# Optimization experiments

Hardware: AMD Instinct MI355X
Metric: run time of the kernel (lower is better)

The kernel has to match this reference:

```python
import jax, jax.numpy as jnp
import numpy as np

H = 256          # NUM_HIDDEN_NODES
D = 2 * H        # encoder feature dim
C_CLS = 1000     # NUM_CLASSES
B = 16
S = 1024
STEPS = 8
WINDOW = 4
MIN_VAL = 1e-8   # min_val global in original


def moving_sum(x, back, fwd):
    # x: [B, T]; sum over window [i-back, i+fwd] (zero padded), as conv1d with ones kernel
    xp = jnp.pad(x, ((0, 0), (back, fwd)))
    k = jnp.ones((1, 1, back + fwd + 1), x.dtype)
    y = jax.lax.conv_general_dilated(xp[:, None, :], k, window_strides=(1,),
                                     padding='VALID', dimension_numbers=('NCH', 'OIH', 'NCH'))
    return y[:, 0, :]


def setup_inputs() -> dict:
    key = jax.random.key(0)
    ks = jax.random.split(key, 24)
    def lin(k, i, o):
        return jax.random.normal(k, (i, o), jnp.float32) * np.float32(1.0 / np.sqrt(i))
    def vec(k, n):
        return jax.random.normal(k, (n,), jnp.float32) * np.float32(1.0 / np.sqrt(n))
    return {
        'enc_output': jax.random.normal(ks[0], (B, S, D), jnp.float32),
        'target': jax.random.randint(ks[1], (B, STEPS), 0, C_CLS),
        'length_enc': jax.random.randint(ks[2], (B,), S // 2, S + 1),
        'noise': jax.random.normal(ks[3], (STEPS, B, S), jnp.float32),
        'Ws_mono_w': lin(ks[4], H, D), 'Ws_mono_b': jnp.zeros((D,), jnp.float32),
        'Wh_mono': lin(ks[5], D, D),
        'v_mono': vec(ks[6], D),
        'g_mono': jnp.full((1,), 1.0 / np.sqrt(D), jnp.float32),
        'r_mono': jnp.full((1,), -4.0, jnp.float32),
        'Ws_chunk_w': lin(ks[7], H, D), 'Ws_chunk_b': jnp.zeros((D,), jnp.float32),
        'Wh_chunk': lin(ks[8], D, D),
        'v_chunk': vec(ks[9], D),
        'L_sy': lin(ks[10], H, H),
        'L_gy_w': lin(ks[11], D, H), 'L_gy_b': jnp.zeros((H,), jnp.float32),
        'L_yy_w': lin(ks[12], H, C_CLS), 'L_yy_b': jnp.zeros((C_CLS,), jnp.float32),
        'L_ys': jax.random.normal(ks[13], (C_CLS, 4 * H), jnp.float32) * 0.02,
        'L_ss': lin(ks[14], H, 4 * H),
        'L_gs_w': lin(ks[15], D, 4 * H), 'L_gs_b': jnp.zeros((4 * H,), jnp.float32),
    }


def reference(enc_output, target, length_enc, noise,
              Ws_mono_w, Ws_mono_b, Wh_mono, v_mono, g_mono, r_mono,
              Ws_chunk_w, Ws_chunk_b, Wh_chunk, v_chunk,
              L_sy, L_gy_w, L_gy_b, L_yy_w, L_yy_b, L_ys, L_ss, L_gs_w, L_gs_b):
    Bn, Sn, _ = enc_output.shape
    Hn = L_sy.shape[0]
    mask = jnp.arange(Sn)[None, :] >= length_enc[:, None]   # True = padded
    neg_inf = jnp.float32(-jnp.inf)
    # step-invariant encoder projections (hoisted out of decode loop)
    enc_mono = enc_output @ Wh_mono     # [B,S,D]
    enc_chunk = enc_output @ Wh_chunk   # [B,S,D]
    v_norm = g_mono[0] / jnp.linalg.norm(v_mono)

    def step(carry, xs):
        s, c, a_prev = carry
        nz, tgt = xs
        # monotonic energies
        tmp1 = jnp.tanh(enc_mono + (s @ Ws_mono_w + Ws_mono_b)[:, None, :])
        e_mono = jnp.einsum('bsd,d->bs', v_norm * tmp1, v_mono) + r_mono[0]
        e_mono = jnp.where(mask, neg_inf, e_mono)
        p = jax.nn.sigmoid(e_mono + nz)
        # monotonic attention recurrence via stable cumsum/cumprod
        logf = jnp.log(jnp.clip(1.0 - p[:, :-1], MIN_VAL, 1.0))
        cpp = jnp.concatenate([jnp.ones((Bn, 1), p.dtype), jnp.exp(jnp.cumsum(logf, axis=1))], axis=1)
        q = cpp * jnp.cumsum(a_prev / jnp.clip(cpp, MIN_VAL, 1.0), axis=1)
        alpha = jnp.clip(p * q, MIN_VAL, 1.0)
        # chunkwise attention
        tmp2 = jnp.tanh(enc_chunk + (s @ Ws_chunk_w + Ws_chunk_b)[:, None, :])
        e_ch = jnp.where(mask, neg_inf, jnp.einsum('bsd,d->bs', tmp2, v_chunk))
        e_ch = e_ch - jnp.max(e_ch, axis=1, keepdims=True)
        ex = jnp.clip(jnp.exp(e_ch), 1e-5, None)
        denom = jnp.clip(moving_sum(ex, WINDOW - 1, 0), 1e-10, None)
        beta = ex * moving_sum(alpha / denom, 0, WINDOW - 1)
        ctx = jnp.einsum('bs,bsd->bd', beta, enc_output)
        # decoder LSTM cell
        rec = L_ys[tgt] + s @ L_ss + ctx @ L_gs_w + L_gs_b
        i, f, g, o = jnp.split(rec, 4, axis=1)
        c_new = jax.nn.sigmoid(f) * c + jax.nn.sigmoid(i) * jnp.tanh(g)
        s_new = jax.nn.sigmoid(o) * jnp.tanh(c_new)
        y = jnp.tanh(ctx @ L_gy_w + L_gy_b + s_new @ L_sy) @ L_yy_w + L_yy_b
        return (s_new, c_new, jax.lax.stop_gradient(alpha)), y

    a0 = jnp.zeros((Bn, Sn), enc_output.dtype).at[:, 0].set(1.0)
    s0 = jnp.zeros((Bn, Hn), enc_output.dtype)
    c0 = jnp.zeros((Bn, Hn), enc_output.dtype)
    _, ys = jax.lax.scan(step, (s0, c0, a0), (noise, target.T))
    return jnp.transpose(ys, (1, 0, 2))   # [B, steps, NUM_CLASSES]
```

## Files before the change

kernel.cpp:

```cpp
#include <hip/hip_runtime.h>
#include <math.h>
#include <float.h>

#define HN 256
#define DN 512
#define CCLS 1000
#define BB 16
#define SS 1024
#define NSTEPS 8
#define G4 1024
#define KV 768

using f16x8 = __attribute__((ext_vector_type(8))) _Float16;
using f32x4 = __attribute__((ext_vector_type(4))) float;

__device__ __forceinline__ void gload_lds16(const void* g, void* l) {
    __builtin_amdgcn_global_load_lds((const __attribute__((address_space(1))) void*)g,
                                     (__attribute__((address_space(3))) void*)l, 16, 0, 0);
}

__device__ __forceinline__ float ftanh(float x) {
    float e = __expf(2.f * x);
    return 1.f - 2.f / (e + 1.f);
}
__device__ __forceinline__ float fsigm(float x) {
    return 1.f / (1.f + __expf(-x));
}

__global__ __launch_bounds__(512) void init_k(const float* __restrict__ vM, const float* __restrict__ g,
                                              const float* __restrict__ Wsmb, const float* __restrict__ Wscb,
                                              float* __restrict__ aA, float* __restrict__ sctxA,
                                              float* __restrict__ cbuf,
                                              float* __restrict__ smb, float* __restrict__ scb,
                                              float* __restrict__ vn) {
    int bid = blockIdx.x, t = threadIdx.x;
    if (bid == 96) {
        __shared__ float red[512];
        float x = vM[t];
        red[t] = x * x;
        __syncthreads();
        for (int off = 256; off > 0; off >>= 1) {
            if (t < off) red[t] += red[t + off];
            __syncthreads();
        }
        if (t == 0) vn[0] = g[0] / sqrtf(red[0]);
        return;
    }
    int i = bid * 512 + t;
    if (i < 16384) {
        aA[i] = ((i & (SS - 1)) == 0) ? 1.f : 0.f;
    } else if (i < 28672) {
        sctxA[i - 16384] = 0.f;
    } else if (i < 32768) {
        cbuf[i - 28672] = 0.f;
    } else if (i < 40960) {
        int j = i - 32768;
        smb[j] = Wsmb[j & (DN - 1)];
    } else {
        int j = i - 40960;
        scb[j] = Wscb[j & (DN - 1)];
    }
}

__global__ __launch_bounds__(256) void conv_enc_k(const float* __restrict__ in,
                                                  _Float16* __restrict__ out) {
    size_t i = ((size_t)blockIdx.x * 256 + threadIdx.x) * 8;
    float4 a = *(const float4*)(in + i);
    float4 b = *(const float4*)(in + i + 4);
    f16x8 o;
    o[0] = (_Float16)a.x; o[1] = (_Float16)a.y; o[2] = (_Float16)a.z; o[3] = (_Float16)a.w;
    o[4] = (_Float16)b.x; o[5] = (_Float16)b.y; o[6] = (_Float16)b.z; o[7] = (_Float16)b.w;
    *(f16x8*)(out + i) = o;
}

__global__ __launch_bounds__(256) void convW_k(const float* __restrict__ W1,
                                               const float* __restrict__ W2,
                                               _Float16* __restrict__ WcT) {
    int kt = blockIdx.x;
    int nt = blockIdx.y;
    __shared__ _Float16 tile[32][33];
    int tx = threadIdx.x & 31, ty = threadIdx.x >> 5;
    int n0 = nt * 32, k0 = kt * 32;
    for (int r = 0; r < 32; r += 8) {
        int k = k0 + ty + r, n = n0 + tx;
        float v = (n < 512) ? W1[(size_t)k * 512 + n] : W2[(size_t)k * 512 + (n - 512)];
        tile[tx][ty + r] = (_Float16)v;
    }
    __syncthreads();
    for (int r = 0; r < 32; r += 8) {
        int n = n0 + ty + r, k = k0 + tx;
        WcT[(size_t)n * 512 + k] = tile[ty + r][tx];
    }
}

__global__ __launch_bounds__(256) void transAll_k(const float* __restrict__ Lss, const float* __restrict__ Lgs,
                                                  const float* __restrict__ Lsy, const float* __restrict__ Lgy,
                                                  const float* __restrict__ Wsm, const float* __restrict__ Wsc,
                                                  const float* __restrict__ Lyy,
                                                  float* __restrict__ WgT, float* __restrict__ WyT,
                                                  float* __restrict__ WpT, float* __restrict__ LyyT) {
    int bid = blockIdx.x;
    const float* src; float* dst; int R, C, dstride, coloff, ctiles;
    if (bid < 256)       { src = Lss; dst = WgT;  R = 256; C = 1024; dstride = KV; coloff = 0;  ctiles = 32; }
    else if (bid < 768)  { src = Lgs; dst = WgT;  R = 512; C = 1024; dstride = KV; coloff = HN; ctiles = 32; bid -= 256; }
    else if (bid < 832)  { src = Lsy; dst = WyT;  R = 256; C = 256;  dstride = KV; coloff = 0;  ctiles = 8;  bid -= 768; }
    else if (bid < 960)  { src = Lgy; dst = WyT;  R = 512; C = 256;  dstride = KV; coloff = HN; ctiles = 8;  bid -= 832; }
    else if (bid < 1088) { src = Wsm; dst = WpT;  R = 256; C = 512;  dstride = HN; coloff = 0;  ctiles = 16; bid -= 960; }
    else if (bid < 1216) { src = Wsc; dst = WpT + (size_t)DN * HN; R = 256; C = 512; dstride = HN; coloff = 0; ctiles = 16; bid -= 1088; }
    else                 { src = Lyy; dst = LyyT; R = 256; C = 1000; dstride = HN; coloff = 0;  ctiles = 32; bid -= 1216; }
    int ct = bid % ctiles, rt = bid / ctiles;
    __shared__ float tile[32][33];
    int c0 = ct * 32, r0 = rt * 32;
    int tx = threadIdx.x & 31, ty = threadIdx.x >> 5;
    for (int rr = 0; rr < 32; rr += 8) {
        int r = r0 + ty + rr, cc = c0 + tx;
        tile[ty + rr][tx] = (r < R && cc < C) ? src[(size_t)r * C + cc] : 0.f;
    }
    __syncthreads();
    for (int rr = 0; rr < 32; rr += 8) {
        int cc = c0 + ty + rr, r = r0 + tx;
        if (cc < C && r < R) dst[(size_t)cc * dstride + coloff + r] = tile[tx][ty + rr];
    }
}

__global__ __launch_bounds__(256) void gemm16_k(const _Float16* __restrict__ A16,
                                                const _Float16* __restrict__ WcT,
                                                _Float16* __restrict__ encMC) {
    __shared__ _Float16 Alds[128 * 32];
    __shared__ _Float16 Blds[128 * 32];
    int bm = blockIdx.x;
    int bn = blockIdx.y;
    int tid = threadIdx.x;
    int lane = tid & 63;
    int w = tid >> 6;
    int wr = w >> 1, wc = w & 1;
    int lr = lane & 15;
    int kg = lane >> 4;
    f32x4 acc[4][4];
#pragma unroll
    for (int i = 0; i < 4; i++)
#pragma unroll
        for (int j = 0; j < 4; j++) acc[i][j] = (f32x4){0.f, 0.f, 0.f, 0.f};

    int wavebase = tid & ~63;
    for (int k0 = 0; k0 < 512; k0 += 32) {
        __syncthreads();
#pragma unroll
        for (int is = 0; is < 2; is++) {
            int l = is * 256 + tid;
            int row = l >> 2, kgs = l & 3;
            int kp = kgs ^ ((row ^ (row >> 2)) & 3);
            gload_lds16(A16 + (size_t)(bm * 128 + row) * 512 + k0 + kp * 8,
                        (char*)Alds + (size_t)(is * 256 + wavebase) * 16);
            gload_lds16(WcT + (size_t)(bn * 128 + row) * 512 + k0 + kp * 8,
                        (char*)Blds + (size_t)(is * 256 + wavebase) * 16);
        }
        __syncthreads();
        f16x8 af[4], bf[4];
#pragma unroll
        for (int mi = 0; mi < 4; mi++) {
            int r = wr * 64 + mi * 16 + lr;
            int kp = kg ^ ((r ^ (r >> 2)) & 3);
            af[mi] = *(const f16x8*)(Alds + r * 32 + kp * 8);
        }
#pragma unroll
        for (int ni = 0; ni < 4; ni++) {
            int cgl = wc * 64 + ni * 16 + lr;
            int kp = kg ^ ((cgl ^ (cgl >> 2)) & 3);
            bf[ni] = *(const f16x8*)(Blds + cgl * 32 + kp * 8);
        }
#pragma unroll
        for (int mi = 0; mi < 4; mi++)
#pragma unroll
            for (int ni = 0; ni < 4; ni++)
                acc[mi][ni] = __builtin_amdgcn_mfma_f32_16x16x32_f16(af[mi], bf[ni], acc[mi][ni], 0, 0, 0);
    }
    int cr = lane >> 4;
#pragma unroll
    for (int mi = 0; mi < 4; mi++)
#pragma unroll
        for (int ni = 0; ni < 4; ni++) {
            int col = bn * 128 + wc * 64 + ni * 16 + lr;
#pragma unroll
            for (int j = 0; j < 4; j++) {
                int row = bm * 128 + wr * 64 + mi * 16 + cr * 4 + j;
                encMC[(size_t)row * 1024 + col] = (_Float16)acc[mi][ni][j];
            }
        }
}

__device__ __forceinline__ void out_proj(int bid2, int tid, float* shbuf,
                                         const float* __restrict__ yv,
                                         const float* __restrict__ LyyT, const float* __restrict__ Lyyb,
                                         float* __restrict__ out, int tt) {
    for (int i = tid * 4; i < BB * HN; i += 1024)
        *(float4*)&shbuf[i] = *(const float4*)&yv[i];
    __syncthreads();
    int wave = tid >> 6, lane = tid & 63;
    int c0 = (bid2 * 4 + wave) * 4;
    for (int q = 0; q < 4; q++) {
        int cc = c0 + q;
        if (cc >= CCLS) break;
        const float* wp = LyyT + (size_t)cc * HN;
        float acc[BB] = {0.f};
#pragma unroll
        for (int k = 0; k < 4; k++) {
            int e = lane + k * 64;
            float wv = wp[e];
#pragma unroll
            for (int b = 0; b < BB; b++) acc[b] = fmaf(wv, shbuf[b * HN + e], acc[b]);
        }
#pragma unroll
        for (int b = 0; b < BB; b++)
#pragma unroll
            for (int off = 32; off > 0; off >>= 1) acc[b] += __shfl_xor(acc[b], off);
        if (lane == 0) {
            float bias = Lyyb[cc];
#pragma unroll
            for (int b = 0; b < BB; b++) out[((size_t)b * NSTEPS + tt) * CCLS + cc] = acc[b] + bias;
        }
    }
}

__global__ __launch_bounds__(256) void energy_out_k(const _Float16* __restrict__ encMC,
                                                    const float* __restrict__ sm, const float* __restrict__ sc,
                                                    const float* __restrict__ vM, const float* __restrict__ vC,
                                                    const float* __restrict__ vnorm, const float* __restrict__ rmono,
                                                    const int* __restrict__ len, const float* __restrict__ noise_t,
                                                    float* __restrict__ p, float* __restrict__ ech,
                                                    const float* __restrict__ yv,
                                                    const float* __restrict__ LyyT, const float* __restrict__ Lyyb,
                                                    float* __restrict__ out, int t) {
    __shared__ float shbuf[BB * HN];
    int tid = threadIdx.x;
    if (blockIdx.x >= 4096) {
        if (t > 0) out_proj(blockIdx.x - 4096, tid, shbuf, yv, LyyT, Lyyb, out, t - 1);
        return;
    }
    int wave = blockIdx.x * 4 + (tid >> 6);
    int lane = tid & 63;
    int b = wave >> 10;
    int si = wave & 1023;
    const f16x8* row = (const f16x8*)(encMC + (size_t)wave * 1024);
    f16x8 em = row[lane];
    f16x8 ec = row[64 + lane];
    int d0 = lane * 8;
    float4 sma = *(const float4*)&sm[b * DN + d0];
    float4 smbv = *(const float4*)&sm[b * DN + d0 + 4];
    float4 sca = *(const float4*)&sc[b * DN + d0];
    float4 scbv = *(const float4*)&sc[b * DN + d0 + 4];
    float4 vma = *(const float4*)&vM[d0];
    float4 vmb = *(const float4*)&vM[d0 + 4];
    float4 vca = *(const float4*)&vC[d0];
    float4 vcb = *(const float4*)&vC[d0 + 4];
    float smv[8] = {sma.x, sma.y, sma.z, sma.w, smbv.x, smbv.y, smbv.z, smbv.w};
    float scv[8] = {sca.x, sca.y, sca.z, sca.w, scbv.x, scbv.y, scbv.z, scbv.w};
    float vmv[8] = {vma.x, vma.y, vma.z, vma.w, vmb.x, vmb.y, vmb.z, vmb.w};
    float vcv[8] = {vca.x, vca.y, vca.z, vca.w, vcb.x, vcb.y, vcb.z, vcb.w};
    float s1 = 0.f, s2 = 0.f;
#pragma unroll
    for (int j = 0; j < 8; j++) {
        s1 += ftanh((float)em[j] + smv[j]) * vmv[j];
        s2 += ftanh((float)ec[j] + scv[j]) * vcv[j];
    }
#pragma unroll
    for (int off = 32; off > 0; off >>= 1) {
        s1 += __shfl_xor(s1, off);
        s2 += __shfl_xor(s2, off);
    }
    if (lane == 0) {
        bool masked = (si >= len[b]);
        float pe;
        if (masked) {
            pe = 0.f;
        } else {
            float e = vnorm[0] * s1 + rmono[0] + noise_t[b * SS + si];
            pe = fsigm(e);
        }
        p[b * SS + si] = pe;
        ech[b * SS + si] = masked ? -INFINITY : s2;
    }
}

__global__ __launch_bounds__(1024) void scanrow_k(const float* __restrict__ p,
                                                  const float* __restrict__ aprev,
                                                  const float* __restrict__ ech,
                                                  float* __restrict__ anew,
                                                  float* __restrict__ beta) {
    int b = blockIdx.x;
    int i = threadIdx.x;
    int lane = i & 63, w = i >> 6;
    __shared__ float wred[16];
    __shared__ float wred2[16];
    __shared__ float mred[16];
    __shared__ float exS[SS];
    __shared__ float rS[SS];
    float pi = p[b * SS + i];
    float lf = (i < SS - 1) ? logf(fminf(fmaxf(1.f - pi, 1e-8f), 1.f)) : 0.f;
    float x = lf;
#pragma unroll
    for (int off = 1; off < 64; off <<= 1) {
        float n = __shfl_up(x, off);
        if (lane >= off) x += n;
    }
    if (lane == 63) wred[w] = x;
    float e = ech[b * SS + i];
    float mx = e;
#pragma unroll
    for (int off = 32; off > 0; off >>= 1) mx = fmaxf(mx, __shfl_xor(mx, off));
    if (lane == 0) mred[w] = mx;
    __syncthreads();
    float base = 0.f;
    for (int j = 0; j < 16; j++)
        if (j < w) base += wred[j];
    float csum = base + x;
    float cpp = expf(csum - lf);
    float u = aprev[b * SS + i] / fminf(fmaxf(cpp, 1e-8f), 1.f);
    float m = mred[0];
    for (int j = 1; j < 16; j++) m = fmaxf(m, mred[j]);
    float x2 = u;
#pragma unroll
    for (int off = 1; off < 64; off <<= 1) {
        float n = __shfl_up(x2, off);
        if (lane >= off) x2 += n;
    }
    if (lane == 63) wred2[w] = x2;
    __syncthreads();
    float base2 = 0.f;
    for (int j = 0; j < 16; j++)
        if (j < w) base2 += wred2[j];
    float q = cpp * (base2 + x2);
    float alpha = fminf(fmaxf(pi * q, 1e-8f), 1.f);
    anew[b * SS + i] = alpha;
    float ex = fmaxf(expf(e - m), 1e-5f);
    exS[i] = ex;
    __syncthreads();
    float denom = ex;
    if (i >= 1) denom += exS[i - 1];
    if (i >= 2) denom += exS[i - 2];
    if (i >= 3) denom += exS[i - 3];
    denom = fmaxf(denom, 1e-10f);
    rS[i] = alpha / denom;
    __syncthreads();
    float bsum = rS[i];
    if (i + 1 < SS) bsum += rS[i + 1];
    if (i + 2 < SS) bsum += rS[i + 2];
    if (i + 3 < SS) bsum += rS[i + 3];
    beta[b * SS + i] = ex * bsum;
}

__global__ __launch_bounds__(512) void ctxpart_k(const float* __restrict__ beta,
                                                 const _Float16* __restrict__ enc16,
                                                 float* __restrict__ part4) {
    int b = blockIdx.x, chunk = blockIdx.y;
    int d = threadIdx.x;
    int s0 = chunk * 256;
    float acc0 = 0.f, acc1 = 0.f;
    const _Float16* eb = enc16 + ((size_t)(b * SS + s0)) * DN + d;
    const float* bb_ = beta + b * SS + s0;
#pragma unroll 4
    for (int s = 0; s < 256; s += 2) {
        acc0 = fmaf(bb_[s], (float)eb[(size_t)s * DN], acc0);
        acc1 = fmaf(bb_[s + 1], (float)eb[(size_t)(s + 1) * DN], acc1);
    }
    part4[((size_t)b * 4 + chunk) * DN + d] = acc0 + acc1;
}

__global__ __launch_bounds__(256) void gl_k(const float* __restrict__ part4,
                                            const float* __restrict__ sIn,
                                            const float* __restrict__ WgT,
                                            const int* __restrict__ target, int t,
                                            const float* __restrict__ Lys, const float* __restrict__ Lgsb,
                                            float* __restrict__ c, float* __restrict__ sOut) {
    __shared__ float sl[BB * KV];
    __shared__ float recL[2][4][BB];
    int tid = threadIdx.x;
    for (int i = tid; i < BB * HN; i += 256) {
        int b = i >> 8, d = i & (HN - 1);
        sl[b * KV + d] = sIn[b * KV + d];
    }
    for (int i = tid; i < BB * DN; i += 256) {
        int b = i >> 9, d = i & (DN - 1);
        const float* pp = part4 + ((size_t)b * 4) * DN + d;
        sl[b * KV + HN + d] = (pp[0] + pp[DN]) + (pp[2 * DN] + pp[3 * DN]);
    }
    __syncthreads();
    int wave = tid >> 6, lane = tid & 63;
    int h0 = blockIdx.x * 2;
    const float* w0p = WgT + (size_t)(h0 + wave * HN) * KV;
    const float* w1p = WgT + (size_t)(h0 + 1 + wave * HN) * KV;
    float acc0[BB] = {0.f}, acc1[BB] = {0.f};
#pragma unroll
    for (int j = 0; j < 12; j++) {
        int e = lane + j * 64;
        float w0 = w0p[e], w1 = w1p[e];
#pragma unroll
        for (int b = 0; b < BB; b++) {
            float xv = sl[b * KV + e];
            acc0[b] = fmaf(w0, xv, acc0[b]);
            acc1[b] = fmaf(w1, xv, acc1[b]);
        }
    }
#pragma unroll
    for (int b = 0; b < BB; b++)
#pragma unroll
        for (int off = 32; off > 0; off >>= 1) {
            acc0[b] += __shfl_xor(acc0[b], off);
            acc1[b] += __shfl_xor(acc1[b], off);
        }
    if (lane == 0) {
#pragma unroll
        for (int b = 0; b < BB; b++) {
            recL[0][wave][b] = acc0[b];
            recL[1][wave][b] = acc1[b];
        }
    }
    __syncthreads();
    if (tid < 32) {
        int b = tid & 15, hh = tid >> 4;
        int h = h0 + hh;
        int tgt = target[b * NSTEPS + t];
        const float* ys = Lys + (size_t)tgt * G4;
        float ri = recL[hh][0][b] + ys[h] + Lgsb[h];
        float rf = recL[hh][1][b] + ys[h + HN] + Lgsb[h + HN];
        float rg = recL[hh][2][b] + ys[h + 2 * HN] + Lgsb[h + 2 * HN];
        float ro = recL[hh][3][b] + ys[h + 3 * HN] + Lgsb[h + 3 * HN];
        float cn = fsigm(rf) * c[b * HN + h] + fsigm(ri) * ftanh(rg);
        float sn = fsigm(ro) * ftanh(cn);
        c[b * HN + h] = cn;
        sOut[b * KV + h] = sn;
    }
    if (blockIdx.x == 0) {
        for (int i = tid; i < BB * DN; i += 256) {
            int b = i >> 9, d = i & (DN - 1);
            sOut[b * KV + HN + d] = sl[b * KV + HN + d];
        }
    }
}

__global__ __launch_bounds__(256) void ypj_k(const float* __restrict__ sctx,
                                             const float* __restrict__ WyT, const float* __restrict__ Lgyb,
                                             const float* __restrict__ WpT,
                                             const float* __restrict__ Wsmb, const float* __restrict__ Wscb,
                                             float* __restrict__ yv,
                                             float* __restrict__ smb, float* __restrict__ scb) {
    __shared__ float sl[BB * KV];
    int tid = threadIdx.x;
    for (int i = tid * 4; i < BB * KV; i += 1024)
        *(float4*)&sl[i] = *(const float4*)&sctx[i];
    __syncthreads();
    int wave = tid >> 6, lane = tid & 63;
    if (blockIdx.x < 16) {
        int h0 = blockIdx.x * 16 + wave * 4;
        for (int q = 0; q < 4; q++) {
            int h = h0 + q;
            const float* wp = WyT + (size_t)h * KV;
            float acc[BB] = {0.f};
#pragma unroll
            for (int j = 0; j < 12; j++) {
                int e = lane + j * 64;
                float wv = wp[e];
#pragma unroll
                for (int b = 0; b < BB; b++) acc[b] = fmaf(wv, sl[b * KV + e], acc[b]);
            }
#pragma unroll
            for (int b = 0; b < BB; b++)
#pragma unroll
                for (int off = 32; off > 0; off >>= 1) acc[b] += __shfl_xor(acc[b], off);
            if (lane == 0) {
#pragma unroll
                for (int b = 0; b < BB; b++) yv[b * HN + h] = ftanh(acc[b] + Lgyb[h]);
            }
        }
    } else {
        int j0 = (blockIdx.x - 16) * 16 + wave * 4;
        for (int q = 0; q < 4; q++) {
            int jc = j0 + q;
            const float* wp = WpT + (size_t)jc * HN;
            float acc[BB] = {0.f};
#pragma unroll
            for (int k = 0; k < 4; k++) {
                int e = lane + k * 64;
                float wv = wp[e];
#pragma unroll
                for (int b = 0; b < BB; b++) acc[b] = fmaf(wv, sl[b * KV + e], acc[b]);
            }
#pragma unroll
            for (int b = 0; b < BB; b++)
#pragma unroll
                for (int off = 32; off > 0; off >>= 1) acc[b] += __shfl_xor(acc[b], off);
            if (lane == 0) {
                if (jc < DN) {
#pragma unroll
                    for (int b = 0; b < BB; b++) smb[b * DN + jc] = acc[b] + Wsmb[jc];
                } else {
                    int jj = jc - DN;
#pragma unroll
                    for (int b = 0; b < BB; b++) scb[b * DN + jj] = acc[b] + Wscb[jj];
                }
            }
        }
    }
}

__global__ __launch_bounds__(256) void out_k(const float* __restrict__ yv,
                                             const float* __restrict__ LyyT, const float* __restrict__ Lyyb,
                                             float* __restrict__ out, int t) {
    __shared__ float shbuf[BB * HN];
    out_proj(blockIdx.x, threadIdx.x, shbuf, yv, LyyT, Lyyb, out, t);
}

extern "C" void kernel_launch(void* const* d_in, const int* in_sizes, int n_in,
                              void* d_out, int out_size, void* d_ws, size_t ws_size,
                              hipStream_t stream) {
    const float* enc  = (const float*)d_in[0];
    const int*   target = (const int*)d_in[1];
    const int*   len  = (const int*)d_in[2];
    const float* noise = (const float*)d_in[3];
    const float* Wsm  = (const float*)d_in[4];
    const float* Wsmb = (const float*)d_in[5];
    const float* WhM  = (const float*)d_in[6];
    const float* vM   = (const float*)d_in[7];
    const float* g    = (const float*)d_in[8];
    const float* rm   = (const float*)d_in[9];
    const float* Wsc  = (const float*)d_in[10];
    const float* Wscb = (const float*)d_in[11];
    const float* WhC  = (const float*)d_in[12];
    const float* vC   = (const float*)d_in[13];
    const float* Lsy  = (const float*)d_in[14];
    const float* Lgy  = (const float*)d_in[15];
    const float* Lgyb = (const float*)d_in[16];
    const float* Lyy  = (const float*)d_in[17];
    const float* Lyyb = (const float*)d_in[18];
    const float* Lys  = (const float*)d_in[19];
    const float* Lss  = (const float*)d_in[20];
    const float* Lgs  = (const float*)d_in[21];
    const float* Lgsb = (const float*)d_in[22];
    float* out = (float*)d_out;

    char* w = (char*)d_ws;
    size_t off = 0;
    auto alloc = [&](size_t bytes) { void* pp = w + off; off += (bytes + 255) & ~(size_t)255; return pp; };
    _Float16* A16   = (_Float16*)alloc((size_t)BB * SS * DN * 2);
    _Float16* WcT   = (_Float16*)alloc((size_t)1024 * 512 * 2);
    _Float16* encMC = (_Float16*)alloc((size_t)BB * SS * 1024 * 2);
    float* WgT  = (float*)alloc((size_t)G4 * KV * 4);
    float* WyT  = (float*)alloc((size_t)HN * KV * 4);
    float* WpT  = (float*)alloc((size_t)G4 * HN * 4);
    float* LyyT = (float*)alloc((size_t)CCLS * HN * 4);
    float* smb   = (float*)alloc(BB * DN * 4);
    float* scb   = (float*)alloc(BB * DN * 4);
    float* pbuf  = (float*)alloc(BB * SS * 4);
    float* ech   = (float*)alloc(BB * SS * 4);
    float* aA    = (float*)alloc(BB * SS * 4);
    float* aBf   = (float*)alloc(BB * SS * 4);
    float* betab = (float*)alloc(BB * SS * 4);
    float* part4 = (float*)alloc((size_t)BB * 4 * DN * 4);
    float* sctxA = (float*)alloc((size_t)BB * KV * 4);
    float* sctxB = (float*)alloc((size_t)BB * KV * 4);
    float* yvb   = (float*)alloc((size_t)BB * HN * 4);
    float* cbuf  = (float*)alloc(BB * HN * 4);
    float* vn    = (float*)alloc(16);
    (void)ws_size; (void)in_sizes; (void)n_in; (void)out_size;

    init_k<<<97, 512, 0, stream>>>(vM, g, Wsmb, Wscb, aA, sctxA, cbuf, smb, scb, vn);
    conv_enc_k<<<4096, 256, 0, stream>>>(enc, A16);
    convW_k<<<dim3(16, 32), 256, 0, stream>>>(WhM, WhC, WcT);
    gemm16_k<<<dim3(128, 8), 256, 0, stream>>>(A16, WcT, encMC);
    transAll_k<<<1472, 256, 0, stream>>>(Lss, Lgs, Lsy, Lgy, Wsm, Wsc, Lyy, WgT, WyT, WpT, LyyT);

    for (int t = 0; t < NSTEPS; t++) {
        float* ain  = (t % 2 == 0) ? aA : aBf;
        float* aout = (t % 2 == 0) ? aBf : aA;
        float* sIn  = (t % 2 == 0) ? sctxA : sctxB;
        float* sOut = (t % 2 == 0) ? sctxB : sctxA;
        energy_out_k<<<4159, 256, 0, stream>>>(encMC, smb, scb, vM, vC, vn, rm,
                                               len, noise + (size_t)t * BB * SS, pbuf, ech,
                                               yvb, LyyT, Lyyb, out, t);
        scanrow_k<<<BB, 1024, 0, stream>>>(pbuf, ain, ech, aout, betab);
        ctxpart_k<<<dim3(BB, 4), 512, 0, stream>>>(betab, A16, part4);
        gl_k<<<128, 256, 0, stream>>>(part4, sIn, WgT, target, t, Lys, Lgsb, cbuf, sOut);
        ypj_k<<<80, 256, 0, stream>>>(sOut, WyT, Lgyb, WpT, Wsmb, Wscb, yvb, smb, scb);
    }
    out_k<<<63, 256, 0, stream>>>(yvb, LyyT, Lyyb, out, NSTEPS - 1);
}
```

Measured before the change: 563.1 us.

## Fuse context reduction into scan kernel and split state/context buffers

Merges the per-step context weighted-sum into the alpha/beta scan kernel, so beta stays in shared memory and one launch plus the partial-sum buffer go away. The hidden state and context are kept in separate buffers, and gl_k is retiled to 512-thread blocks computing four hidden units each. The fused reduction runs on only 16 blocks with long sequential loops over the sequence, which lowers parallelism for that stage.

New measurement: 768.0 us. 36.4% more time.

```diff
diff --git a/kernel.cpp b/kernel.cpp
--- a/kernel.cpp
+++ b/kernel.cpp
@@ -29,12 +29,12 @@
 
 __global__ __launch_bounds__(512) void init_k(const float* __restrict__ vM, const float* __restrict__ g,
                                               const float* __restrict__ Wsmb, const float* __restrict__ Wscb,
-                                              float* __restrict__ aA, float* __restrict__ sctxA,
+                                              float* __restrict__ aA, float* __restrict__ sA,
                                               float* __restrict__ cbuf,
                                               float* __restrict__ smb, float* __restrict__ scb,
                                               float* __restrict__ vn) {
     int bid = blockIdx.x, t = threadIdx.x;
-    if (bid == 96) {
+    if (bid == 80) {
         __shared__ float red[512];
         float x = vM[t];
         red[t] = x * x;
@@ -49,15 +49,15 @@
     int i = bid * 512 + t;
     if (i < 16384) {
         aA[i] = ((i & (SS - 1)) == 0) ? 1.f : 0.f;
-    } else if (i < 28672) {
-        sctxA[i - 16384] = 0.f;
+    } else if (i < 20480) {
+        sA[i - 16384] = 0.f;
+    } else if (i < 24576) {
+        cbuf[i - 20480] = 0.f;
     } else if (i < 32768) {
-        cbuf[i - 28672] = 0.f;
-    } else if (i < 40960) {
-        int j = i - 32768;
+        int j = i - 24576;
         smb[j] = Wsmb[j & (DN - 1)];
     } else {
-        int j = i - 40960;
+        int j = i - 32768;
         scb[j] = Wscb[j & (DN - 1)];
     }
 }
@@ -141,7 +141,6 @@
     for (int i = 0; i < 4; i++)
 #pragma unroll
         for (int j = 0; j < 4; j++) acc[i][j] = (f32x4){0.f, 0.f, 0.f, 0.f};
-
     int wavebase = tid & ~63;
     for (int k0 = 0; k0 < 512; k0 += 32) {
         __syncthreads();
@@ -270,23 +269,19 @@
     }
     if (lane == 0) {
         bool masked = (si >= len[b]);
-        float pe;
-        if (masked) {
-            pe = 0.f;
-        } else {
-            float e = vnorm[0] * s1 + rmono[0] + noise_t[b * SS + si];
-            pe = fsigm(e);
-        }
+        float pe = 0.f;
+        if (!masked) pe = fsigm(vnorm[0] * s1 + rmono[0] + noise_t[b * SS + si]);
         p[b * SS + si] = pe;
         ech[b * SS + si] = masked ? -INFINITY : s2;
     }
 }
 
-__global__ __launch_bounds__(1024) void scanrow_k(const float* __restrict__ p,
+__global__ __launch_bounds__(1024) void scanctx_k(const float* __restrict__ p,
                                                   const float* __restrict__ aprev,
                                                   const float* __restrict__ ech,
+                                                  const _Float16* __restrict__ enc16,
                                                   float* __restrict__ anew,
-                                                  float* __restrict__ beta) {
+                                                  float* __restrict__ ctxbuf) {
     int b = blockIdx.x;
     int i = threadIdx.x;
     int lane = i & 63, w = i >> 6;
@@ -295,6 +290,8 @@
     __shared__ float mred[16];
     __shared__ float exS[SS];
     __shared__ float rS[SS];
+    __shared__ float bS[SS];
+    __shared__ float ctmp[1024];
     float pi = p[b * SS + i];
     float lf = (i < SS - 1) ? logf(fminf(fmaxf(1.f - pi, 1e-8f), 1.f)) : 0.f;
     float x = lf;
@@ -346,49 +343,38 @@
     if (i + 1 < SS) bsum += rS[i + 1];
     if (i + 2 < SS) bsum += rS[i + 2];
     if (i + 3 < SS) bsum += rS[i + 3];
-    beta[b * SS + i] = ex * bsum;
-}
-
-__global__ __launch_bounds__(512) void ctxpart_k(const float* __restrict__ beta,
-                                                 const _Float16* __restrict__ enc16,
-                                                 float* __restrict__ part4) {
-    int b = blockIdx.x, chunk = blockIdx.y;
-    int d = threadIdx.x;
-    int s0 = chunk * 256;
-    float acc0 = 0.f, acc1 = 0.f;
-    const _Float16* eb = enc16 + ((size_t)(b * SS + s0)) * DN + d;
-    const float* bb_ = beta + b * SS + s0;
+    bS[i] = ex * bsum;
+    __syncthreads();
+    int d = i & 511, half = i >> 9;
+    const _Float16* eb = enc16 + ((size_t)(b * SS + half * 512)) * DN + d;
+    const float* bp = bS + half * 512;
+    float acc = 0.f;
 #pragma unroll 4
-    for (int s = 0; s < 256; s += 2) {
-        acc0 = fmaf(bb_[s], (float)eb[(size_t)s * DN], acc0);
-        acc1 = fmaf(bb_[s + 1], (float)eb[(size_t)(s + 1) * DN], acc1);
-    }
-    part4[((size_t)b * 4 + chunk) * DN + d] = acc0 + acc1;
-}
-
-__global__ __launch_bounds__(256) void gl_k(const float* __restrict__ part4,
+    for (int s = 0; s < 512; s++) acc = fmaf(bp[s], (float)eb[(size_t)s * DN], acc);
+    ctmp[i] = acc;
+    __syncthreads();
+    if (i < 512) ctxbuf[b * DN + i] = ctmp[i] + ctmp[i + 512];
+}
+
+__global__ __launch_bounds__(512) void gl_k(const float* __restrict__ ctxbuf,
                                             const float* __restrict__ sIn,
                                             const float* __restrict__ WgT,
                                             const int* __restrict__ target, int t,
                                             const float* __restrict__ Lys, const float* __restrict__ Lgsb,
                                             float* __restrict__ c, float* __restrict__ sOut) {
-    __shared__ float sl[BB * KV];
-    __shared__ float recL[2][4][BB];
+    __shared__ float xl[BB * KV];
+    __shared__ float recL[16][BB];
     int tid = threadIdx.x;
-    for (int i = tid; i < BB * HN; i += 256) {
-        int b = i >> 8, d = i & (HN - 1);
-        sl[b * KV + d] = sIn[b * KV + d];
-    }
-    for (int i = tid; i < BB * DN; i += 256) {
-        int b = i >> 9, d = i & (DN - 1);
-        const float* pp = part4 + ((size_t)b * 4) * DN + d;
-        sl[b * KV + HN + d] = (pp[0] + pp[DN]) + (pp[2 * DN] + pp[3 * DN]);
-    }
-    __syncthreads();
-    int wave = tid >> 6, lane = tid & 63;
-    int h0 = blockIdx.x * 2;
-    const float* w0p = WgT + (size_t)(h0 + wave * HN) * KV;
-    const float* w1p = WgT + (size_t)(h0 + 1 + wave * HN) * KV;
+    for (int i = tid; i < BB * HN; i += 512)
+        xl[(i >> 8) * KV + (i & (HN - 1))] = sIn[i];
+    for (int i = tid; i < BB * DN; i += 512)
+        xl[(i >> 9) * KV + HN + (i & (DN - 1))] = ctxbuf[i];
+    __syncthreads();
+    int wv = tid >> 6, lane = tid & 63;
+    int h0 = blockIdx.x * 4;
+    int ri0 = wv * 2, ri1 = ri0 + 1;
+    const float* w0p = WgT + (size_t)((ri0 >> 2) * HN + h0 + (ri0 & 3)) * KV;
+    const float* w1p = WgT + (size_t)((ri1 >> 2) * HN + h0 + (ri1 & 3)) * KV;
     float acc0[BB] = {0.f}, acc1[BB] = {0.f};
 #pragma unroll
     for (int j = 0; j < 12; j++) {
@@ -396,7 +382,7 @@
         float w0 = w0p[e], w1 = w1p[e];
 #pragma unroll
         for (int b = 0; b < BB; b++) {
-            float xv = sl[b * KV + e];
+            float xv = xl[b * KV + e];
             acc0[b] = fmaf(w0, xv, acc0[b]);
             acc1[b] = fmaf(w1, xv, acc1[b]);
         }
@@ -411,34 +397,29 @@
     if (lane == 0) {
 #pragma unroll
         for (int b = 0; b < BB; b++) {
-            recL[0][wave][b] = acc0[b];
-            recL[1][wave][b] = acc1[b];
-        }
-    }
-    __syncthreads();
-    if (tid < 32) {
+            recL[ri0][b] = acc0[b];
+            recL[ri1][b] = acc1[b];
+        }
+    }
+    __syncthreads();
+    if (tid < 64) {
         int b = tid & 15, hh = tid >> 4;
         int h = h0 + hh;
         int tgt = target[b * NSTEPS + t];
         const float* ys = Lys + (size_t)tgt * G4;
-        float ri = recL[hh][0][b] + ys[h] + Lgsb[h];
-        float rf = recL[hh][1][b] + ys[h + HN] + Lgsb[h + HN];
-        float rg = recL[hh][2][b] + ys[h + 2 * HN] + Lgsb[h + 2 * HN];
-        float ro = recL[hh][3][b] + ys[h + 3 * HN] + Lgsb[h + 3 * HN];
+        float ri = recL[0 * 4 + hh][b] + ys[h] + Lgsb[h];
+        float rf = recL[1 * 4 + hh][b] + ys[h + HN] + Lgsb[h + HN];
+        float rg = recL[2 * 4 + hh][b] + ys[h + 2 * HN] + Lgsb[h + 2 * HN];
+        float ro = recL[3 * 4 + hh][b] + ys[h + 3 * HN] + Lgsb[h + 3 * HN];
         float cn = fsigm(rf) * c[b * HN + h] + fsigm(ri) * ftanh(rg);
         float sn = fsigm(ro) * ftanh(cn);
         c[b * HN + h] = cn;
-        sOut[b * KV + h] = sn;
-    }
-    if (blockIdx.x == 0) {
-        for (int i = tid; i < BB * DN; i += 256) {
-            int b = i >> 9, d = i & (DN - 1);
-            sOut[b * KV + HN + d] = sl[b * KV + HN + d];
-        }
-    }
-}
-
-__global__ __launch_bounds__(256) void ypj_k(const float* __restrict__ sctx,
+        sOut[b * HN + h] = sn;
+    }
+}
+
+__global__ __launch_bounds__(256) void ypj_k(const float* __restrict__ sNew,
+                                             const float* __restrict__ ctxbuf,
                                              const float* __restrict__ WyT, const float* __restrict__ Lgyb,
                                              const float* __restrict__ WpT,
                                              const float* __restrict__ Wsmb, const float* __restrict__ Wscb,
@@ -446,8 +427,10 @@
                                              float* __restrict__ smb, float* __restrict__ scb) {
     __shared__ float sl[BB * KV];
     int tid = threadIdx.x;
-    for (int i = tid * 4; i < BB * KV; i += 1024)
-        *(float4*)&sl[i] = *(const float4*)&sctx[i];
+    for (int i = tid; i < BB * HN; i += 256)
+        sl[(i >> 8) * KV + (i & (HN - 1))] = sNew[i];
+    for (int i = tid; i < BB * DN; i += 256)
+        sl[(i >> 9) * KV + HN + (i & (DN - 1))] = ctxbuf[i];
     __syncthreads();
     int wave = tid >> 6, lane = tid & 63;
     if (blockIdx.x < 16) {
@@ -554,16 +537,15 @@
     float* ech   = (float*)alloc(BB * SS * 4);
     float* aA    = (float*)alloc(BB * SS * 4);
     float* aBf   = (float*)alloc(BB * SS * 4);
-    float* betab = (float*)alloc(BB * SS * 4);
-    float* part4 = (float*)alloc((size_t)BB * 4 * DN * 4);
-    float* sctxA = (float*)alloc((size_t)BB * KV * 4);
-    float* sctxB = (float*)alloc((size_t)BB * KV * 4);
+    float* ctxbuf = (float*)alloc((size_t)BB * DN * 4);
+    float* sA    = (float*)alloc((size_t)BB * HN * 4);
+    float* sB    = (float*)alloc((size_t)BB * HN * 4);
     float* yvb   = (float*)alloc((size_t)BB * HN * 4);
     float* cbuf  = (float*)alloc(BB * HN * 4);
     float* vn    = (float*)alloc(16);
     (void)ws_size; (void)in_sizes; (void)n_in; (void)out_size;
 
-    init_k<<<97, 512, 0, stream>>>(vM, g, Wsmb, Wscb, aA, sctxA, cbuf, smb, scb, vn);
+    init_k<<<81, 512, 0, stream>>>(vM, g, Wsmb, Wscb, aA, sA, cbuf, smb, scb, vn);
     conv_enc_k<<<4096, 256, 0, stream>>>(enc, A16);
     convW_k<<<dim3(16, 32), 256, 0, stream>>>(WhM, WhC, WcT);
     gemm16_k<<<dim3(128, 8), 256, 0, stream>>>(A16, WcT, encMC);
@@ -572,15 +554,14 @@
     for (int t = 0; t < NSTEPS; t++) {
         float* ain  = (t % 2 == 0) ? aA : aBf;
         float* aout = (t % 2 == 0) ? aBf : aA;
-        float* sIn  = (t % 2 == 0) ? sctxA : sctxB;
-        float* sOut = (t % 2 == 0) ? sctxB : sctxA;
+        float* sIn  = (t % 2 == 0) ? sA : sB;
+        float* sOut = (t % 2 == 0) ? sB : sA;
         energy_out_k<<<4159, 256, 0, stream>>>(encMC, smb, scb, vM, vC, vn, rm,
                                                len, noise + (size_t)t * BB * SS, pbuf, ech,
                                                yvb, LyyT, Lyyb, out, t);
-        scanrow_k<<<BB, 1024, 0, stream>>>(pbuf, ain, ech, aout, betab);
-        ctxpart_k<<<dim3(BB, 4), 512, 0, stream>>>(betab, A16, part4);
-        gl_k<<<128, 256, 0, stream>>>(part4, sIn, WgT, target, t, Lys, Lgsb, cbuf, sOut);
-        ypj_k<<<80, 256, 0, stream>>>(sOut, WyT, Lgyb, WpT, Wsmb, Wscb, yvb, smb, scb);
+        scanctx_k<<<BB, 1024, 0, stream>>>(pbuf, ain, ech, A16, aout, ctxbuf);
+        gl_k<<<64, 512, 0, stream>>>(ctxbuf, sIn, WgT, target, t, Lys, Lgsb, cbuf, sOut);
+        ypj_k<<<80, 256, 0, stream>>>(sOut, ctxbuf, WyT, Lgyb, WpT, Wsmb, Wscb, yvb, smb, scb);
     }
     out_k<<<63, 256, 0, stream>>>(yvb, LyyT, Lyyb, out, NSTEPS - 1);
 }
```
